# Kernel optimization log

Measured on AMD Instinct MI355X. Metric: run time of the kernel, lower is better.

Reference implementation:

```python
import jax, jax.numpy as jnp
import numpy as np

NE = 20000      # num_ents
NR = 250        # num_rels
R2 = 2 * NR     # num_rels * 2
H = 256         # h_dim
T = 3           # sequence_len (history length)
E = 150000      # edges per timestep
M = 200000      # r_to_e entries per timestep
NNZ_E = 320000  # hypergraph-ent nnz
NNZ_R = 8000    # hypergraph-rel nnz
NLH_E = 2       # n_layers_hypergraph_ent
NLH_R = 2       # n_layers_hypergraph_rel
CH = 50         # ConvTransE channels
NT = 2000       # test triples (doubled with inverses)


def seg_mean(vals, ids, n):
    s = jax.ops.segment_sum(vals, ids, num_segments=n)
    c = jax.ops.segment_sum(jnp.ones((ids.shape[0], 1), vals.dtype), ids, num_segments=n)
    return s / jnp.maximum(c, 1.0)


def l2norm(x, eps=1e-12):  # F.normalize(dim=1)
    n = jnp.linalg.norm(x, axis=-1, keepdims=True)
    return x / jnp.maximum(n, eps)


def gru_cell(x, h, W_ih, W_hh, b_ih, b_hh):  # torch.nn.GRUCell math
    gi = x @ W_ih.T + b_ih
    gh = h @ W_hh.T + b_hh
    i_r, i_z, i_n = jnp.split(gi, 3, axis=-1)
    h_r, h_z, h_n = jnp.split(gh, 3, axis=-1)
    r = jax.nn.sigmoid(i_r + h_r)
    z = jax.nn.sigmoid(i_z + h_z)
    n = jnp.tanh(i_n + r * h_n)
    return (1.0 - z) * n + z * h


def setup_inputs() -> dict:
    key = jax.random.key(0)
    ks = jax.random.split(key, 32)
    inp = {}
    inp['dynamic_emb'] = jax.random.normal(ks[0], (NE, H), jnp.float32)
    inp['emb_rel'] = jax.random.normal(ks[1], (R2, H), jnp.float32) * 0.06
    inp['gru_W_ih'] = jax.random.normal(ks[2], (3 * H, 2 * H), jnp.float32) * 0.05
    inp['gru_W_hh'] = jax.random.normal(ks[3], (3 * H, H), jnp.float32) * 0.05
    inp['gru_b_ih'] = jnp.zeros((3 * H,), jnp.float32)
    inp['gru_b_hh'] = jnp.zeros((3 * H,), jnp.float32)
    inp['agg_W'] = jax.random.normal(ks[4], (H, H), jnp.float32) * 0.06
    inp['tg_W'] = jax.random.normal(ks[5], (H, H), jnp.float32) * 0.06
    inp['tg_b'] = jnp.zeros((H,), jnp.float32)
    inp['hyper_ent_val'] = jax.random.uniform(ks[6], (NNZ_E,), jnp.float32) * (1.0 / 16.0)
    inp['hyper_rel_val'] = jax.random.uniform(ks[7], (NNZ_R,), jnp.float32) * (1.0 / 16.0)
    inp['conv_w'] = jax.random.normal(ks[8], (CH, 3, 3), jnp.float32) * 0.1
    inp['conv_b'] = jnp.zeros((CH,), jnp.float32)
    inp['fc_W'] = jax.random.normal(ks[9], (CH * H, H), jnp.float32) * 0.01
    inp['fc_b'] = jnp.zeros((H,), jnp.float32)
    inp['sentence_emb'] = jax.random.normal(ks[10], (NT, H), jnp.float32)
    inp['edge_src'] = jax.random.randint(ks[11], (T, E), 0, NE, jnp.int64)
    inp['edge_rel'] = jax.random.randint(ks[12], (T, E), 0, R2, jnp.int64)
    inp['edge_dst'] = jax.random.randint(ks[13], (T, E), 0, NE, jnp.int64)
    inp['r_to_e'] = jax.random.randint(ks[14], (T, M), 0, NE, jnp.int64)
    inp['r_ids'] = jax.random.randint(ks[15], (T, M), 0, R2, jnp.int64)
    inp['hyper_ent_row'] = jax.random.randint(ks[16], (NNZ_E,), 0, NE, jnp.int64)
    inp['hyper_ent_col'] = jax.random.randint(ks[17], (NNZ_E,), 0, NE, jnp.int64)
    inp['hyper_rel_row'] = jax.random.randint(ks[18], (NNZ_R,), 0, R2, jnp.int64)
    inp['hyper_rel_col'] = jax.random.randint(ks[19], (NNZ_R,), 0, R2, jnp.int64)
    inp['test_triples'] = jax.random.randint(ks[20], (NT, 3), 0, NR, jnp.int64)
    return inp


def reference(dynamic_emb, emb_rel, gru_W_ih, gru_W_hh, gru_b_ih, gru_b_hh,
              agg_W, tg_W, tg_b, hyper_ent_val, hyper_rel_val,
              conv_w, conv_b, fc_W, fc_b, sentence_emb,
              edge_src, edge_rel, edge_dst, r_to_e, r_ids,
              hyper_ent_row, hyper_ent_col, hyper_rel_row, hyper_rel_col,
              test_triples):
    ent = dynamic_emb   # [NE, H]  (layer_norm=False -> no normalize)
    rel = emb_rel       # [R2, H]
    # --- temporal evolution over history (sequence_len timesteps) ---
    for t in range(T):
        # per-relation gather-mean of involved entity embeddings (r_to_e spans)
        x_mean = seg_mean(ent[r_to_e[t]], r_ids[t], R2)          # [R2, H]
        x_in = jnp.concatenate([rel, x_mean], axis=1)             # [R2, 2H]
        rel = gru_cell(x_in, rel, gru_W_ih, gru_W_hh, gru_b_ih, gru_b_hh)
        # aggregator: relational message passing (mean over in-edges)
        msg = (ent[edge_src[t]] + rel[edge_rel[t]]) @ agg_W       # [E, H]
        curr = jax.nn.relu(seg_mean(msg, edge_dst[t], NE))        # [NE, H]
        # time gate
        tw = jax.nn.sigmoid(ent @ tg_W + tg_b)
        ent = tw * curr + (1.0 - tw) * ent
    # --- hypergraph propagation (sparse spmv + L2 normalize + residual) ---
    x = ent
    for _ in range(NLH_E):
        y = jax.ops.segment_sum(hyper_ent_val[:, None] * x[hyper_ent_col],
                                hyper_ent_row, num_segments=NE)
        x = l2norm(y) + x
    ent = x
    x = rel
    for _ in range(NLH_R):
        y = jax.ops.segment_sum(hyper_rel_val[:, None] * x[hyper_rel_col],
                                hyper_rel_row, num_segments=R2)
        x = l2norm(y) + x
    rel = x
    # --- predict: add inverse triples, ConvTransE decoder ---
    inv = jnp.stack([test_triples[:, 2], test_triples[:, 1] + NR, test_triples[:, 0]], axis=1)
    all_t = jnp.concatenate([test_triples, inv], axis=0)          # [2NT, 3]
    sent = jnp.concatenate([sentence_emb, sentence_emb], axis=0)  # [2NT, H]
    e1 = ent[all_t[:, 0]]
    r1 = rel[all_t[:, 1]]
    feat = jnp.stack([e1, r1, sent], axis=1)                      # [B, 3, H]
    conv = jax.lax.conv_general_dilated(feat, conv_w, window_strides=(1,),
                                        padding=((1, 1),),
                                        dimension_numbers=('NCH', 'OIH', 'NCH'))
    conv = jax.nn.relu(conv + conv_b[None, :, None])              # [B, CH, H]
    q = jax.nn.relu(conv.reshape(feat.shape[0], CH * H) @ fc_W + fc_b)  # [B, H]
    scores = q @ ent.T                                            # [B, NE]
    # cross-entropy over object entity
    tgt = all_t[:, 2]
    logz = jax.scipy.special.logsumexp(scores, axis=1)
    nll = logz - jnp.take_along_axis(scores, tgt[:, None], axis=1)[:, 0]
    return jnp.mean(nll)
```

## Files before the change

### kernel.cpp

```cpp
#include <hip/hip_runtime.h>
#include <math.h>

#define DEV_INLINE __device__ __forceinline__

constexpr int H      = 256;
constexpr int NE     = 20000;
constexpr int NR     = 250;
constexpr int R2     = 500;
constexpr int TT     = 3;
constexpr int NEDGE  = 150000;
constexpr int M      = 200000;
constexpr int NNZ_E  = 320000;
constexpr int NNZ_R  = 8000;
constexpr int CH     = 50;
constexpr int NT     = 2000;
constexpr int NT2    = 4000;
constexpr int H3     = 3 * H;
constexpr int KFC    = CH * H;
constexpr int ROWPAD = 4096;
constexpr int NCHUNK = 32;
constexpr int SPP    = 20;
constexpr int MSPLIT = 8;
constexpr int FSPLIT = 20;
constexpr int NB_CS  = 64;
constexpr int NEPAD  = 20480;
constexpr int NB_NE  = 80;
constexpr float PADCOLS = 480.f;

constexpr int CNT_NE_BASE   = 2048;
constexpr int CNT_NE_STRIDE = 20224;
constexpr int CNT_TOTAL     = CNT_NE_BASE + 4 * CNT_NE_STRIDE;

typedef __bf16 bf16x8 __attribute__((ext_vector_type(8)));
typedef float  f32x4  __attribute__((ext_vector_type(4)));

DEV_INLINE bf16x8 ldb8(const __bf16* p) { return *(const bf16x8*)p; }
DEV_INLINE bf16x8 zerob8() { uint4 z = make_uint4(0, 0, 0, 0); return __builtin_bit_cast(bf16x8, z); }
DEV_INLINE f32x4 mfma16(bf16x8 a, bf16x8 b, f32x4 c) {
  return __builtin_amdgcn_mfma_f32_16x16x32_bf16(a, b, c, 0, 0, 0);
}
DEV_INLINE void gload_lds16(const void* g, void* l) {
  __builtin_amdgcn_global_load_lds((const __attribute__((address_space(1))) void*)g,
                                   (__attribute__((address_space(3))) void*)l, 16, 0, 0);
}

DEV_INLINE float block_sum256(float v) {
  __shared__ float ws[4];
  #pragma unroll
  for (int o = 32; o > 0; o >>= 1) v += __shfl_down(v, o, 64);
  if ((threadIdx.x & 63) == 0) ws[threadIdx.x >> 6] = v;
  __syncthreads();
  float r = ws[0] + ws[1] + ws[2] + ws[3];
  __syncthreads();
  return r;
}

__global__ void cs_hist_k(const int* __restrict__ r_ids, const int* __restrict__ hr_row,
                          int* __restrict__ bcnt)
{
  __shared__ int lh[512];
  int a = blockIdx.y;
  const int* keys = (a < 3) ? r_ids + (size_t)a * M : hr_row;
  int n = (a < 3) ? M : NNZ_R;
  int t = threadIdx.x;
  lh[t] = 0; lh[t + 256] = 0;
  __syncthreads();
  int chunk = (n + NB_CS - 1) / NB_CS;
  int i0 = blockIdx.x * chunk, i1 = min(i0 + chunk, n);
  for (int i = i0 + t; i < i1; i += 256) atomicAdd(&lh[keys[i]], 1);
  __syncthreads();
  int* outp = bcnt + ((size_t)a * NB_CS + blockIdx.x) * 512;
  outp[t] = lh[t]; outp[t + 256] = lh[t + 256];
}

__global__ void cs_scan_k(const int* __restrict__ bcnt, int* __restrict__ bbase,
                          int* __restrict__ start_all)
{
  __shared__ int ps[257];
  int a = blockIdx.x;
  int* start = start_all + ((a < 3) ? a * 512 : 1536);
  const int* bc = bcnt + (size_t)a * NB_CS * 512;
  int* bb = bbase + (size_t)a * NB_CS * 512;
  int t = threadIdx.x;
  int b0 = 2 * t, b1 = 2 * t + 1;
  int tot0 = 0, tot1 = 0;
  for (int blk = 0; blk < NB_CS; blk++) {
    tot0 += bc[blk * 512 + b0];
    tot1 += bc[blk * 512 + b1];
  }
  ps[t + 1] = tot0 + tot1;
  if (t == 0) ps[0] = 0;
  __syncthreads();
  if (t == 0) { for (int i = 1; i <= 256; i++) ps[i] += ps[i - 1]; }
  __syncthreads();
  int run0 = ps[t], run1 = ps[t] + tot0;
  start[b0] = run0;
  start[b1] = run1;
  for (int blk = 0; blk < NB_CS; blk++) {
    bb[blk * 512 + b0] = run0; run0 += bc[blk * 512 + b0];
    bb[blk * 512 + b1] = run1; run1 += bc[blk * 512 + b1];
  }
}

__global__ void cs_scatter_k(const int* __restrict__ r_ids, const int* __restrict__ r_to_e,
                             const int* __restrict__ hr_row, const int* __restrict__ hr_col,
                             const float* __restrict__ hrv, const int* __restrict__ bbase,
                             int* __restrict__ f0, int* __restrict__ f1, int* __restrict__ f2,
                             int2* __restrict__ fcvHR)
{
  __shared__ int cur[512];
  int a = blockIdx.y;
  const int* keys = (a < 3) ? r_ids + (size_t)a * M : hr_row;
  int n = (a < 3) ? M : NNZ_R;
  int t = threadIdx.x;
  const int* bb = bbase + ((size_t)a * NB_CS + blockIdx.x) * 512;
  cur[t] = bb[t]; cur[t + 256] = bb[t + 256];
  __syncthreads();
  int chunk = (n + NB_CS - 1) / NB_CS;
  int i0 = blockIdx.x * chunk, i1 = min(i0 + chunk, n);
  if (a < 3) {
    const int* other = r_to_e + (size_t)a * M;
    int* f = (a == 0) ? f0 : (a == 1) ? f1 : f2;
    for (int i = i0 + t; i < i1; i += 256) {
      int p = atomicAdd(&cur[keys[i]], 1);
      f[p] = other[i];
    }
  } else {
    for (int i = i0 + t; i < i1; i += 256) {
      int p = atomicAdd(&cur[keys[i]], 1);
      fcvHR[p] = make_int2(hr_col[i], __float_as_int(hrv[i]));
    }
  }
}

__global__ void hist_ne_k(const int* __restrict__ edge_dst, const int* __restrict__ he_row,
                          int* __restrict__ cnt_all)
{
  int a = blockIdx.y;
  const int* keys = (a < 3) ? edge_dst + (size_t)a * NEDGE : he_row;
  int n = (a < 3) ? NEDGE : NNZ_E;
  int* cnt = cnt_all + CNT_NE_BASE + a * CNT_NE_STRIDE;
  int i = blockIdx.x * 256 + threadIdx.x;
  if (i < n) atomicAdd(&cnt[keys[i]], 1);
}

__global__ void scan_ne1_k(const int* __restrict__ cnt_all, int* __restrict__ start_all,
                           int* __restrict__ bsum)
{
  __shared__ int wtot[4];
  int a = blockIdx.y;
  int off = CNT_NE_BASE + a * CNT_NE_STRIDE;
  int bin = blockIdx.x * 256 + threadIdx.x;
  int lane = threadIdx.x & 63, w = threadIdx.x >> 6;
  int v = (bin < NE) ? cnt_all[off + bin] : 0;
  int orig = v;
  #pragma unroll
  for (int o = 1; o < 64; o <<= 1) {
    int n = __shfl_up(v, o, 64);
    if (lane >= o) v += n;
  }
  if (lane == 63) wtot[w] = v;
  __syncthreads();
  int wo = 0;
  #pragma unroll
  for (int i = 0; i < 4; i++) if (i < w) wo += wtot[i];
  if (bin < NE) start_all[off + bin] = v - orig + wo;
  if (threadIdx.x == 255) bsum[a * NB_NE + blockIdx.x] = wo + v;
}

__global__ void scan_ne2_k(int* __restrict__ bsum, int* __restrict__ start_all)
{
  __shared__ int s[NB_NE + 1];
  int a = blockIdx.x;
  int t = threadIdx.x;
  if (t < NB_NE) s[t + 1] = bsum[a * NB_NE + t];
  if (t == 0) s[0] = 0;
  __syncthreads();
  if (t == 0) { for (int i = 1; i <= NB_NE; i++) s[i] += s[i - 1]; }
  __syncthreads();
  if (t < NB_NE) bsum[a * NB_NE + t] = s[t];
  if (t == 0) start_all[CNT_NE_BASE + a * CNT_NE_STRIDE + NE] = s[NB_NE];
}

__global__ void scan_ne3_k(int* __restrict__ start_all, int* __restrict__ cursor_all,
                           const int* __restrict__ bsum)
{
  int a = blockIdx.y;
  int off = CNT_NE_BASE + a * CNT_NE_STRIDE;
  int bin = blockIdx.x * 256 + threadIdx.x;
  if (bin >= NE) return;
  int v = start_all[off + bin] + bsum[a * NB_NE + blockIdx.x];
  start_all[off + bin] = v;
  cursor_all[off + bin] = v;
}

__global__ void perm_fuse2i_k(const int* __restrict__ edge_dst, const int* __restrict__ edge_src,
                              const int* __restrict__ edge_rel, int* __restrict__ cursor_all,
                              int2* __restrict__ f0, int2* __restrict__ f1, int2* __restrict__ f2)
{
  int a = blockIdx.y;
  const int* keys = edge_dst + (size_t)a * NEDGE;
  const int* o1 = edge_src + (size_t)a * NEDGE;
  const int* o2 = edge_rel + (size_t)a * NEDGE;
  int* cursor = cursor_all + CNT_NE_BASE + a * CNT_NE_STRIDE;
  int2* f = (a == 0) ? f0 : (a == 1) ? f1 : f2;
  int i = blockIdx.x * 256 + threadIdx.x;
  if (i < NEDGE) { int p = atomicAdd(&cursor[keys[i]], 1); f[p] = make_int2(o1[i], o2[i]); }
}
__global__ void perm_fusevi_k(const int* __restrict__ keys, const int* __restrict__ col,
                              const float* __restrict__ val, int n, int* __restrict__ cursor,
                              int2* __restrict__ f)
{
  int i = blockIdx.x * 256 + threadIdx.x;
  if (i < n) {
    int p = atomicAdd(&cursor[keys[i]], 1);
    f[p] = make_int2(col[i], __float_as_int(val[i]));
  }
}

__global__ void cast_bf16_k(const float* __restrict__ in, __bf16* __restrict__ out, int n8)
{
  int i = blockIdx.x * 256 + threadIdx.x;
  if (i >= n8) return;
  const float4* p = (const float4*)in + (size_t)i * 2;
  float4 u = p[0], v = p[1];
  bf16x8 o;
  o[0] = (__bf16)u.x; o[1] = (__bf16)u.y; o[2] = (__bf16)u.z; o[3] = (__bf16)u.w;
  o[4] = (__bf16)v.x; o[5] = (__bf16)v.y; o[6] = (__bf16)v.z; o[7] = (__bf16)v.w;
  ((bf16x8*)out)[i] = o;
}

__global__ void copy_cast_k(const float* __restrict__ in, float* __restrict__ outf,
                            __bf16* __restrict__ outb, int n8)
{
  int i = blockIdx.x * 256 + threadIdx.x;
  if (i >= n8) return;
  const float4* p = (const float4*)in + (size_t)i * 2;
  float4 u = p[0], v = p[1];
  ((float4*)outf)[(size_t)i * 2]     = u;
  ((float4*)outf)[(size_t)i * 2 + 1] = v;
  bf16x8 o;
  o[0] = (__bf16)u.x; o[1] = (__bf16)u.y; o[2] = (__bf16)u.z; o[3] = (__bf16)u.w;
  o[4] = (__bf16)v.x; o[5] = (__bf16)v.y; o[6] = (__bf16)v.z; o[7] = (__bf16)v.w;
  ((bf16x8*)outb)[i] = o;
}

__global__ void transpose_cast_k(const float* __restrict__ in, __bf16* __restrict__ out,
                                 int K, int N)
{
  __shared__ float tile[32][33];
  int tx = threadIdx.x & 31, ty = threadIdx.x >> 5;
  int kb = blockIdx.x * 32, nb = blockIdx.y * 32;
  #pragma unroll
  for (int i = 0; i < 4; i++)
    tile[ty + i * 8][tx] = in[(size_t)(kb + ty + i * 8) * N + nb + tx];
  __syncthreads();
  #pragma unroll
  for (int i = 0; i < 4; i++)
    out[(size_t)(nb + ty + i * 8) * K + kb + tx] = (__bf16)tile[tx][ty + i * 8];
}

__global__ void pack_frag_k(const __bf16* __restrict__ src, __bf16* __restrict__ dst,
                            int nchunks, int Mr)
{
  int i = blockIdx.x * 256 + threadIdx.x;
  if (i >= nchunks) return;
  int c = i >> 5, s = i & 31;
  bf16x8 v = (c < Mr) ? ldb8(src + (size_t)c * H + s * 8) : zerob8();
  int kf = s >> 2, kg = s & 3;
  size_t d = ((((size_t)(c >> 6) * 4 + ((c >> 4) & 3)) * 8 + kf) * 4 + kg) * 16 + (c & 15);
  *(bf16x8*)(dst + d * 8) = v;
}

__global__ void gather_mean2_k(const __bf16* __restrict__ src, const int* __restrict__ fidx,
                               const int* __restrict__ start, float* __restrict__ part)
{
  __shared__ __align__(16) float red[4][H];
  int r = blockIdx.x, s = blockIdx.y;
  int s0 = start[r], s1 = start[r + 1];
  int len = s1 - s0;
  int chunk = (len + MSPLIT - 1) / MSPLIT;
  int jb = s0 + s * chunk, je = min(jb + chunk, s1);
  int tid = threadIdx.x, lane = tid & 63, w = tid >> 6;
  int half = lane >> 5, l = lane & 31;
  float acc[8] = {0.f, 0.f, 0.f, 0.f, 0.f, 0.f, 0.f, 0.f};
  for (int j = jb + w * 2 + half; j < je; j += 8) {
    int e = fidx[j];
    bf16x8 v = ldb8(src + (size_t)e * H + l * 8);
    #pragma unroll
    for (int q = 0; q < 8; q++) acc[q] += (float)v[q];
  }
  #pragma unroll
  for (int q = 0; q < 8; q++) acc[q] += __shfl_xor(acc[q], 32, 64);
  if (half == 0) {
    *(float4*)&red[w][l * 8]     = make_float4(acc[0], acc[1], acc[2], acc[3]);
    *(float4*)&red[w][l * 8 + 4] = make_float4(acc[4], acc[5], acc[6], acc[7]);
  }
  __syncthreads();
  int h = tid;
  part[((size_t)r * MSPLIT + s) * H + h] = red[0][h] + red[1][h] + red[2][h] + red[3][h];
}

__global__ void mean_xin_k(const float* __restrict__ partM, const int* __restrict__ start,
                           const float* __restrict__ rel, __bf16* __restrict__ xin)
{
  int r = blockIdx.x, h = threadIdx.x;
  float s = 0.f;
  #pragma unroll
  for (int z = 0; z < MSPLIT; z++) s += partM[((size_t)r * MSPLIT + z) * H + h];
  float xm = s / (float)max(start[r + 1] - start[r], 1);
  xin[(size_t)r * 2 * H + h]     = (__bf16)rel[(size_t)r * H + h];
  xin[(size_t)r * 2 * H + H + h] = (__bf16)xm;
}

__global__ void gather_edges3_k(const __bf16* __restrict__ ent, const __bf16* __restrict__ rel,
                                const int2* __restrict__ fsr,
                                const int* __restrict__ start, __bf16* __restrict__ out)
{
  __shared__ __align__(16) float red[4][H];
  int d = blockIdx.x;
  int s0 = start[d], s1 = start[d + 1];
  int tid = threadIdx.x, lane = tid & 63, w = tid >> 6;
  int half = lane >> 5, l = lane & 31;
  const __bf16* srcbase = half ? rel : ent;
  float acc[8] = {0.f, 0.f, 0.f, 0.f, 0.f, 0.f, 0.f, 0.f};
  for (int j = s0 + w; j < s1; j += 4) {
    int2 e2 = fsr[j];
    int e = half ? e2.y : e2.x;
    bf16x8 v = ldb8(srcbase + (size_t)e * H + l * 8);
    #pragma unroll
    for (int q = 0; q < 8; q++) acc[q] += (float)v[q];
  }
  #pragma unroll
  for (int q = 0; q < 8; q++) acc[q] += __shfl_xor(acc[q], 32, 64);
  if (half == 0) {
    *(float4*)&red[w][l * 8]     = make_float4(acc[0], acc[1], acc[2], acc[3]);
    *(float4*)&red[w][l * 8 + 4] = make_float4(acc[4], acc[5], acc[6], acc[7]);
  }
  __syncthreads();
  int h = tid;
  float sum = red[0][h] + red[1][h] + red[2][h] + red[3][h];
  out[(size_t)d * H + h] = (__bf16)(sum / (float)max(s1 - s0, 1));
}

__global__ void hyper3_k(const float* __restrict__ x, const __bf16* __restrict__ xb,
                         const int2* __restrict__ fcv,
                         const int* __restrict__ start,
                         float* __restrict__ xout, __bf16* __restrict__ xoutb)
{
  __shared__ __align__(16) float red[4][H];
  int r = blockIdx.x;
  int s0 = start[r], s1 = start[r + 1];
  int tid = threadIdx.x, lane = tid & 63, w = tid >> 6;
  int half = lane >> 5, l = lane & 31;
  float acc[8] = {0.f, 0.f, 0.f, 0.f, 0.f, 0.f, 0.f, 0.f};
  for (int j = s0 + w * 2 + half; j < s1; j += 8) {
    int2 cv = fcv[j];
    float wt = __int_as_float(cv.y);
    bf16x8 v = ldb8(xb + (size_t)cv.x * H + l * 8);
    #pragma unroll
    for (int q = 0; q < 8; q++) acc[q] += wt * (float)v[q];
  }
  #pragma unroll
  for (int q = 0; q < 8; q++) acc[q] += __shfl_xor(acc[q], 32, 64);
  if (half == 0) {
    *(float4*)&red[w][l * 8]     = make_float4(acc[0], acc[1], acc[2], acc[3]);
    *(float4*)&red[w][l * 8 + 4] = make_float4(acc[4], acc[5], acc[6], acc[7]);
  }
  __syncthreads();
  int h = tid;
  float y = red[0][h] + red[1][h] + red[2][h] + red[3][h];
  float ss = block_sum256(y * y);
  float rn = 1.f / fmaxf(sqrtf(ss), 1e-12f);
  float o = x[(size_t)r * H + h] + y * rn;
  xout[(size_t)r * H + h] = o;
  xoutb[(size_t)r * H + h] = (__bf16)o;
}

__global__ void hyper_rel_k(const float* __restrict__ x, const int2* __restrict__ fcv,
                            const int* __restrict__ start, float* __restrict__ xout)
{
  int r = blockIdx.x, h = threadIdx.x;
  int s0 = start[r], s1 = start[r + 1];
  float a0 = 0.f;
  for (int j = s0; j < s1; j++) {
    int2 cv = fcv[j];
    a0 += __int_as_float(cv.y) * x[(size_t)cv.x * H + h];
  }
  float ss = block_sum256(a0 * a0);
  float rn = 1.f / fmaxf(sqrtf(ss), 1e-12f);
  xout[(size_t)r * H + h] = x[(size_t)r * H + h] + a0 * rn;
}

__global__ void gru_combine(const float* __restrict__ gi, const float* __restrict__ gh,
                            float* __restrict__ rel, __bf16* __restrict__ relb)
{
  int idx = blockIdx.x * 256 + threadIdx.x;
  if (idx >= R2 * H) return;
  int i = idx >> 8, h = idx & 255;
  const float* gir = gi + (size_t)i * H3;
  const float* ghr = gh + (size_t)i * H3;
  float r = 1.f / (1.f + __expf(-(gir[h]       + ghr[h])));
  float z = 1.f / (1.f + __expf(-(gir[H + h]   + ghr[H + h])));
  float n = tanhf(gir[2 * H + h] + r * ghr[2 * H + h]);
  float o = (1.f - z) * n + z * rel[idx];
  rel[idx] = o;
  relb[idx] = (__bf16)o;
}

DEV_INLINE void stage64_load(uint4* v, const __bf16* src, int rowBase, int rowLimit, int tid)
{
  #pragma unroll
  for (int q = 0; q < 8; q++) {
    int X = (q * 256 + tid) * 16;
    int row = X >> 9, boff = X & 511;
    int grow = min(rowBase + row, rowLimit);
    v[q] = *(const uint4*)((const char*)src + (size_t)grow * 512 + boff);
  }
}
DEV_INLINE void stage64_write(char* lds, const uint4* v, int tid)
{
  #pragma unroll
  for (int q = 0; q < 8; q++) {
    int X = (q * 256 + tid) * 16;
    int row = X >> 9;
    *(uint4*)(lds + (X ^ ((row & 7) << 4))) = v[q];
  }
}
DEV_INLINE bf16x8 frag64(const char* lds, int row, int kf, int kg)
{
  int off = (kf * 64 + kg * 16) ^ ((row & 7) << 4);
  return *(const bf16x8*)(lds + row * 512 + off);
}

template<int EPI>
__global__ __launch_bounds__(256, 2) void panel2_gemm(const __bf16* __restrict__ A,
                                                      const __bf16* __restrict__ B,
                                                      const float* __restrict__ bias,
                                                      float* __restrict__ out,
                                                      int Mr, int N,
                                                      const float* __restrict__ gate,
                                                      float* __restrict__ entf,
                                                      __bf16* __restrict__ entbo)
{
  __shared__ __attribute__((aligned(16))) char lds0[32768];
  __shared__ __attribute__((aligned(16))) char lds1[32768];
  int tid = threadIdx.x;
  int lane = tid & 63, wM = tid >> 6;
  int r = lane & 15, kg = lane >> 4;
  int rowBase = blockIdx.y * 128;

  {
    uint4 va[8];
    stage64_load(va, A, rowBase, Mr - 1, tid);
    stage64_write(lds0, va, tid);
    stage64_load(va, A, rowBase + 64, Mr - 1, tid);
    stage64_write(lds1, va, tid);
  }
  __syncthreads();

  bf16x8 a[2][8];
  {
    int base = wM * 32;
    const char* ab = (base >= 64) ? lds1 : lds0;
    #pragma unroll
    for (int i = 0; i < 2; i++) {
      int ar = (base + i * 16 + r) & 63;
      #pragma unroll
      for (int kf = 0; kf < 8; kf++) a[i][kf] = frag64(ab, ar, kf, kg);
    }
  }
  __syncthreads();
  {
    uint4 va[8];
    stage64_load(va, B, blockIdx.x * 64, N - 1, tid);
    stage64_write(lds0, va, tid);
  }
  __syncthreads();

  f32x4 acc[2][4];
  #pragma unroll
  for (int i = 0; i < 2; i++)
    #pragma unroll
    for (int j = 0; j < 4; j++) {
      acc[i][j][0] = 0.f; acc[i][j][1] = 0.f; acc[i][j][2] = 0.f; acc[i][j][3] = 0.f;
    }
  __builtin_amdgcn_s_setprio(1);
  #pragma unroll
  for (int kf = 0; kf < 8; kf++) {
    bf16x8 b[4];
    #pragma unroll
    for (int j = 0; j < 4; j++) b[j] = frag64(lds0, j * 16 + r, kf, kg);
    #pragma unroll
    for (int i = 0; i < 2; i++)
      #pragma unroll
      for (int j = 0; j < 4; j++)
        acc[i][j] = mfma16(a[i][kf], b[j], acc[i][j]);
  }
  __builtin_amdgcn_s_setprio(0);

  #pragma unroll
  for (int i = 0; i < 2; i++)
    #pragma unroll
    for (int g = 0; g < 4; g++) {
      int row = rowBase + wM * 32 + i * 16 + kg * 4 + g;
      if (row >= Mr) continue;
      #pragma unroll
      for (int j = 0; j < 4; j++) {
        int col = blockIdx.x * 64 + j * 16 + r;
        if (col >= N) continue;
        float v = acc[i][j][g];
        if (EPI == 2) {
          if (bias) v += bias[col];
          v = 1.f / (1.f + __expf(-v));
          out[(size_t)row * N + col] = v;
        } else {
          v = fmaxf(v, 0.f);
          size_t idx = (size_t)row * N + col;
          float t = gate[idx];
          float o = t * v + (1.f - t) * entf[idx];
          entf[idx] = o;
          entbo[idx] = (__bf16)o;
        }
      }
    }
}

__global__ __launch_bounds__(256, 3) void scores_v4(const __bf16* __restrict__ qbf,
                                                    const __bf16* __restrict__ ebf,
                                                    float* __restrict__ part_l)
{
  __shared__ __attribute__((aligned(16))) char lds[2][16384];
  int tid = threadIdx.x, lane = tid & 63, w = tid >> 6;
  int r = lane & 15, kg = lane >> 4;

  auto stage = [&](int buf, int p) {
    const char* g = (const char*)ebf + ((size_t)(blockIdx.x * SPP + p)) * 16384;
    int wbase = (tid & ~63) * 16;
    #pragma unroll
    for (int q = 0; q < 4; q++) {
      int o = q * 4096 + wbase;
      gload_lds16(g + o + lane * 16, lds[buf] + o);
    }
  };

  stage(0, 0);

  bf16x8 a[2][8];
  {
    int cb = blockIdx.y * 2 + (w >> 1);
    int jb = (w & 1) * 2;
    const __bf16* ap = qbf + (size_t)cb * 16384 + kg * 128 + r * 8;
    #pragma unroll
    for (int i = 0; i < 2; i++)
      #pragma unroll
      for (int kf = 0; kf < 8; kf++)
        a[i][kf] = ldb8(ap + ((jb + i) * 8 + kf) * 512);
  }
  __syncthreads();

  float lsum[2][4];
  #pragma unroll
  for (int i = 0; i < 2; i++)
    #pragma unroll
    for (int g = 0; g < 4; g++) lsum[i][g] = 0.f;

  const char* l0 = lds[0] + kg * 256 + r * 16;
  const char* l1 = lds[1] + kg * 256 + r * 16;

  for (int p = 0; p < SPP; p++) {
    if (p + 1 < SPP) stage((p + 1) & 1, p + 1);
    const char* cur = (p & 1) ? l1 : l0;

    f32x4 acc[2][2];
    #pragma unroll
    for (int i = 0; i < 2; i++)
      #pragma unroll
      for (int j = 0; j < 2; j++) {
        acc[i][j][0] = 0.f; acc[i][j][1] = 0.f; acc[i][j][2] = 0.f; acc[i][j][3] = 0.f;
      }
    __builtin_amdgcn_s_setprio(1);
    #pragma unroll
    for (int kf = 0; kf < 8; kf++) {
      bf16x8 b0 = *(const bf16x8*)(cur + (0 * 8 + kf) * 1024);
      bf16x8 b1 = *(const bf16x8*)(cur + (1 * 8 + kf) * 1024);
      acc[0][0] = mfma16(a[0][kf], b0, acc[0][0]);
      acc[0][1] = mfma16(a[0][kf], b1, acc[0][1]);
      acc[1][0] = mfma16(a[1][kf], b0, acc[1][0]);
      acc[1][1] = mfma16(a[1][kf], b1, acc[1][1]);
    }
    __builtin_amdgcn_s_setprio(0);

    #pragma unroll
    for (int j = 0; j < 2; j++)
      #pragma unroll
      for (int i = 0; i < 2; i++)
        #pragma unroll
        for (int g = 0; g < 4; g++)
          lsum[i][g] += exp2f(acc[i][j][g]);
    __syncthreads();
  }

  #pragma unroll
  for (int m = 1; m < 16; m <<= 1)
    #pragma unroll
    for (int i = 0; i < 2; i++)
      #pragma unroll
      for (int g = 0; g < 4; g++)
        lsum[i][g] += __shfl_xor(lsum[i][g], m, 64);
  if (r == 0) {
    #pragma unroll
    for (int i = 0; i < 2; i++)
      #pragma unroll
      for (int g = 0; g < 4; g++) {
        int row = blockIdx.y * 128 + w * 32 + i * 16 + kg * 4 + g;
        part_l[(size_t)blockIdx.x * ROWPAD + row] = lsum[i][g];
      }
  }
}

__global__ __launch_bounds__(256) void fc_gemm(const __bf16* __restrict__ A,
                                               const __bf16* __restrict__ Bt,
                                               float* __restrict__ part, int Mr)
{
  __shared__ __attribute__((aligned(16))) char lds[49152];
  int tid = threadIdx.x;
  int lane = tid & 63, wave = tid >> 6;
  int wM = wave >> 1, wN = wave & 1;
  int r = lane & 15, kg = lane >> 4;
  int rowBase = blockIdx.y * 128;
  int kbeg = blockIdx.x * (KFC / FSPLIT);

  f32x4 acc[4][8];
  #pragma unroll
  for (int i = 0; i < 4; i++)
    #pragma unroll
    for (int j = 0; j < 8; j++) {
      acc[i][j][0] = 0.f; acc[i][j][1] = 0.f; acc[i][j][2] = 0.f; acc[i][j][3] = 0.f;
    }

  for (int ks = 0; ks < KFC / FSPLIT / 64; ks++) {
    int kb = kbeg + ks * 64;
    #pragma unroll
    for (int q = 0; q < 12; q++) {
      int X = (q * 256 + tid) * 16;
      int row = X >> 7;
      int off = X & 127;
      int soff = off ^ ((row & 7) << 4);
      uint4 v;
      if (row < 128) {
        int grow = min(rowBase + row, Mr - 1);
        v = *(const uint4*)((const char*)A + (size_t)grow * (KFC * 2) + kb * 2 + soff);
      } else {
        int col = row - 128;
        v = *(const uint4*)((const char*)Bt + (size_t)col * (KFC * 2) + kb * 2 + soff);
      }
      *(uint4*)(lds + X) = v;
    }
    __syncthreads();
    #pragma unroll
    for (int kf = 0; kf < 2; kf++) {
      bf16x8 a[4], b[8];
      #pragma unroll
      for (int i = 0; i < 4; i++) {
        int row = wM * 64 + i * 16 + r;
        int off = (kf * 64 + kg * 16) ^ ((row & 7) << 4);
        a[i] = *(const bf16x8*)(lds + row * 128 + off);
      }
      #pragma unroll
      for (int j = 0; j < 8; j++) {
        int row = 128 + wN * 128 + j * 16 + r;
        int off = (kf * 64 + kg * 16) ^ ((row & 7) << 4);
        b[j] = *(const bf16x8*)(lds + row * 128 + off);
      }
      #pragma unroll
      for (int i = 0; i < 4; i++)
        #pragma unroll
        for (int j = 0; j < 8; j++)
          acc[i][j] = mfma16(a[i], b[j], acc[i][j]);
    }
    __syncthreads();
  }

  float* pz = part + (size_t)blockIdx.x * Mr * H;
  #pragma unroll
  for (int i = 0; i < 4; i++)
    #pragma unroll
    for (int g = 0; g < 4; g++) {
      int row = rowBase + wM * 64 + i * 16 + kg * 4 + g;
      if (row >= Mr) continue;
      #pragma unroll
      for (int j = 0; j < 8; j++) {
        int col = wN * 128 + j * 16 + r;
        pz[(size_t)row * H + col] = acc[i][j][g];
      }
    }
}

__global__ void gru_gemm2_k(const __bf16* __restrict__ xinb, const __bf16* __restrict__ relb,
                            const __bf16* __restrict__ Wihb, const __bf16* __restrict__ Whhb,
                            const float* __restrict__ b_ih, const float* __restrict__ b_hh,
                            float* __restrict__ gi, float* __restrict__ gh)
{
  const __bf16* A; const __bf16* Bt; const float* bias; float* C; int K;
  if (blockIdx.z == 0) { A = xinb; Bt = Wihb; bias = b_ih; C = gi; K = 2 * H; }
  else                 { A = relb; Bt = Whhb; bias = b_hh; C = gh; K = H; }
  const int Mr = R2, N = H3;

  int lane = threadIdx.x & 63, wave = threadIdx.x >> 6;
  int waveM = wave >> 1, waveN = wave & 1;
  int r = lane & 15, kg = lane >> 4;
  int rowBase = blockIdx.y * 64 + waveM * 32;
  int colBase = blockIdx.x * 64 + waveN * 32;

  int row0 = rowBase + r, row1 = rowBase + 16 + r;
  int col0 = colBase + r, col1 = colBase + 16 + r;
  bool v0 = row0 < Mr, v1 = row1 < Mr;
  const __bf16* a0p = A + (size_t)row0 * K + kg * 8;
  const __bf16* a1p = A + (size_t)row1 * K + kg * 8;
  const __bf16* b0p = Bt + (size_t)col0 * K + kg * 8;
  const __bf16* b1p = Bt + (size_t)col1 * K + kg * 8;

  f32x4 acc[2][2];
  #pragma unroll
  for (int i = 0; i < 2; i++)
    #pragma unroll
    for (int j = 0; j < 2; j++) { acc[i][j][0] = 0.f; acc[i][j][1] = 0.f; acc[i][j][2] = 0.f; acc[i][j][3] = 0.f; }

  for (int k0 = 0; k0 < K; k0 += 32) {
    bf16x8 a0 = v0 ? ldb8(a0p + k0) : zerob8();
    bf16x8 a1 = v1 ? ldb8(a1p + k0) : zerob8();
    bf16x8 b0 = ldb8(b0p + k0);
    bf16x8 b1 = ldb8(b1p + k0);
    acc[0][0] = mfma16(a0, b0, acc[0][0]);
    acc[0][1] = mfma16(a0, b1, acc[0][1]);
    acc[1][0] = mfma16(a1, b0, acc[1][0]);
    acc[1][1] = mfma16(a1, b1, acc[1][1]);
  }

  #pragma unroll
  for (int i = 0; i < 2; i++) {
    #pragma unroll
    for (int g = 0; g < 4; g++) {
      int row = rowBase + i * 16 + kg * 4 + g;
      if (row >= Mr) continue;
      #pragma unroll
      for (int j = 0; j < 2; j++) {
        int col = colBase + j * 16 + r;
        C[(size_t)row * N + col] = acc[i][j][g] + bias[col];
      }
    }
  }
}

__global__ void fc_reduce(const float* __restrict__ part, const float* __restrict__ bias,
                          float* __restrict__ q, __bf16* __restrict__ qb, int nrows)
{
  int idx = blockIdx.x * 256 + threadIdx.x;
  if (idx >= nrows * H) return;
  int col = idx & 255;
  float s = bias[col];
  for (int z = 0; z < FSPLIT; z++) s += part[(size_t)z * nrows * H + idx];
  s = fmaxf(s, 0.f);
  q[idx] = s;
  qb[idx] = (__bf16)(s * 1.44269504f);
}

__global__ void conv_feat(const float* __restrict__ ent, const float* __restrict__ rel,
                          const float* __restrict__ sent, const int* __restrict__ tt,
                          const float* __restrict__ cw, const float* __restrict__ cb,
                          __bf16* __restrict__ out, int row0)
{
  __shared__ float f[3][258];
  __shared__ float wsm[CH * 9];
  __shared__ float bsm[CH];
  int i = row0 + blockIdx.x;
  int h = threadIdx.x;
  int j = (i < NT) ? i : i - NT;
  int a0 = (i < NT) ? tt[j * 3 + 0] : tt[j * 3 + 2];
  int a1 = (i < NT) ? tt[j * 3 + 1] : tt[j * 3 + 1] + NR;
  f[0][h + 1] = ent[(size_t)a0 * H + h];
  f[1][h + 1] = rel[(size_t)a1 * H + h];
  f[2][h + 1] = sent[(size_t)j * H + h];
  if (h < 3) { f[h][0] = 0.f; f[h][257] = 0.f; }
  for (int x = h; x < CH * 9; x += 256) wsm[x] = cw[x];
  if (h < CH) bsm[h] = cb[h];
  __syncthreads();
  __bf16* orow = out + (size_t)blockIdx.x * KFC;
  for (int c = 0; c < CH; c++) {
    const float* wc = wsm + c * 9;
    float s = bsm[c];
    #pragma unroll
    for (int ic = 0; ic < 3; ic++)
      s += wc[ic * 3 + 0] * f[ic][h] + wc[ic * 3 + 1] * f[ic][h + 1] + wc[ic * 3 + 2] * f[ic][h + 2];
    orow[(size_t)c * H + h] = (__bf16)fmaxf(s, 0.f);
  }
}

__global__ void lse_combine(const float* __restrict__ part_l, const float* __restrict__ qf,
                            const float* __restrict__ ent, const int* __restrict__ tt,
                            float* __restrict__ nll)
{
  int gid = blockIdx.x * 256 + threadIdx.x;
  int w = gid >> 6;
  if (w >= NT2) return;
  int lane = gid & 63;
  int j = (w < NT) ? w : w - NT;
  int tgt = (w < NT) ? tt[j * 3 + 2] : tt[j * 3 + 0];
  const float4 qa = ((const float4*)(qf + (size_t)w * H))[lane];
  const float4 ea = ((const float4*)(ent + (size_t)tgt * H))[lane];
  float d = qa.x * ea.x + qa.y * ea.y + qa.z * ea.z + qa.w * ea.w;
  float s = (lane < NCHUNK) ? part_l[(size_t)lane * ROWPAD + w] : 0.f;
  #pragma unroll
  for (int o = 32; o > 0; o >>= 1) {
    d += __shfl_down(d, o, 64);
    s += __shfl_down(s, o, 64);
  }
  if (lane == 0) nll[w] = logf(s - PADCOLS) - d;
}

__global__ void mean_nll(const float* __restrict__ nll, float* __restrict__ out)
{
  float s = 0.f;
  for (int i = threadIdx.x; i < NT2; i += 256) s += nll[i];
  s = block_sum256(s);
  if (threadIdx.x == 0) out[0] = s * (1.f / NT2);
}

extern "C" void kernel_launch(void* const* d_in, const int* in_sizes, int n_in,
                              void* d_out, int out_size, void* d_ws, size_t ws_size,
                              hipStream_t stream)
{
  const float* dynamic_emb = (const float*)d_in[0];
  const float* emb_rel     = (const float*)d_in[1];
  const float* gru_W_ih    = (const float*)d_in[2];
  const float* gru_W_hh    = (const float*)d_in[3];
  const float* gru_b_ih    = (const float*)d_in[4];
  const float* gru_b_hh    = (const float*)d_in[5];
  const float* agg_W       = (const float*)d_in[6];
  const float* tg_W        = (const float*)d_in[7];
  const float* tg_b        = (const float*)d_in[8];
  const float* hev         = (const float*)d_in[9];
  const float* hrv         = (const float*)d_in[10];
  const float* conv_w      = (const float*)d_in[11];
  const float* conv_b      = (const float*)d_in[12];
  const float* fc_W        = (const float*)d_in[13];
  const float* fc_b        = (const float*)d_in[14];
  const float* sent        = (const float*)d_in[15];
  const int* edge_src = (const int*)d_in[16];
  const int* edge_rel = (const int*)d_in[17];
  const int* edge_dst = (const int*)d_in[18];
  const int* r_to_e   = (const int*)d_in[19];
  const int* r_ids    = (const int*)d_in[20];
  const int* he_row   = (const int*)d_in[21];
  const int* he_col   = (const int*)d_in[22];
  const int* hr_row   = (const int*)d_in[23];
  const int* hr_col   = (const int*)d_in[24];
  const int* tt       = (const int*)d_in[25];
  float* out = (float*)d_out;

  char* base = (char*)d_ws;
  size_t off = 0;
  auto alloc = [&](size_t bytes) { char* p = base + off; off += (bytes + 255) & ~(size_t)255; return p; };

  float* ent    = (float*)alloc((size_t)NE * H * 4);
  float* curr   = (float*)alloc((size_t)NE * H * 4);
  float* tgbuf  = (float*)alloc((size_t)NE * H * 4);
  __bf16* convb = (__bf16*)curr;
  __bf16* entb  = (__bf16*)alloc((size_t)NE * H * 2);
  __bf16* entb2 = (__bf16*)alloc((size_t)NE * H * 2);
  __bf16* accEb = (__bf16*)alloc((size_t)NE * H * 2);
  __bf16* ebf   = (__bf16*)alloc((size_t)NEPAD * H * 2);
  __bf16* qbf   = (__bf16*)alloc((size_t)ROWPAD * H * 2);
  float* rel    = (float*)alloc((size_t)R2 * H * 4);
  float* accR   = (float*)alloc((size_t)R2 * H * 4);
  __bf16* relb  = (__bf16*)alloc((size_t)R2 * H * 2);
  __bf16* xinb  = (__bf16*)alloc((size_t)R2 * 2 * H * 2);
  float* gi     = (float*)alloc((size_t)R2 * H3 * 4);
  float* gh     = (float*)alloc((size_t)R2 * H3 * 4);
  float* qf     = (float*)alloc((size_t)NT2 * H * 4);
  __bf16* qb    = (__bf16*)alloc((size_t)NT2 * H * 2);
  float* part_l = (float*)alloc((size_t)NCHUNK * ROWPAD * 4);
  float* partM  = (float*)alloc((size_t)R2 * MSPLIT * H * 4);
  float* fcpart = (float*)alloc((size_t)FSPLIT * 1600 * H * 4);
  float* nll    = (float*)alloc((size_t)NT2 * 4);
  __bf16* tgWtb = (__bf16*)alloc((size_t)H * H * 2);
  __bf16* aggWtb= (__bf16*)alloc((size_t)H * H * 2);
  __bf16* fcWtb = (__bf16*)alloc((size_t)H * KFC * 2);
  __bf16* Wihb  = (__bf16*)alloc((size_t)H3 * 2 * H * 2);
  __bf16* Whhb  = (__bf16*)alloc((size_t)H3 * H * 2);

  int* ip = (int*)alloc(0);
  size_t ioff = 0;
  auto ialloc = [&](size_t n) { int* p = ip + ioff; ioff += n; return p; };
  int* fidxM[TT];
  int2* fsrE[TT];
  for (int t = 0; t < TT; t++) fidxM[t] = ialloc(M);
  for (int t = 0; t < TT; t++) fsrE[t] = (int2*)ialloc((size_t)NEDGE * 2);
  int2* fcvHE = (int2*)ialloc((size_t)NNZ_E * 2);
  int2* fcvHR = (int2*)ialloc((size_t)NNZ_R * 2);
  int* cnt_all    = ialloc(CNT_TOTAL);
  int* start_all  = ialloc(CNT_TOTAL);
  int* cursor_all = ialloc(CNT_TOTAL);
  int* bcnt  = ialloc((size_t)4 * NB_CS * 512);
  int* bbase = ialloc((size_t)4 * NB_CS * 512);
  int* bsumNE = ialloc((size_t)4 * NB_NE);

  int* sM[TT];  for (int t = 0; t < TT; t++) sM[t] = start_all + t * 512;
  int* sHR = start_all + 1536;
  int* sE[TT];  for (int t = 0; t < TT; t++) sE[t] = start_all + CNT_NE_BASE + t * CNT_NE_STRIDE;
  int* sHE = start_all + CNT_NE_BASE + 3 * CNT_NE_STRIDE;

  transpose_cast_k<<<dim3(H / 32, H / 32), 256, 0, stream>>>(tg_W, tgWtb, H, H);
  transpose_cast_k<<<dim3(H / 32, H / 32), 256, 0, stream>>>(agg_W, aggWtb, H, H);
  transpose_cast_k<<<dim3(KFC / 32, H / 32), 256, 0, stream>>>(fc_W, fcWtb, KFC, H);
  cast_bf16_k<<<(H3 * 2 * H / 8 + 255) / 256, 256, 0, stream>>>(gru_W_ih, Wihb, H3 * 2 * H / 8);
  cast_bf16_k<<<(H3 * H / 8 + 255) / 256, 256, 0, stream>>>(gru_W_hh, Whhb, H3 * H / 8);

  cs_hist_k<<<dim3(NB_CS, 4), 256, 0, stream>>>(r_ids, hr_row, bcnt);
  cs_scan_k<<<4, 256, 0, stream>>>(bcnt, bbase, start_all);
  cs_scatter_k<<<dim3(NB_CS, 4), 256, 0, stream>>>(r_ids, r_to_e, hr_row, hr_col, hrv, bbase,
                                                   fidxM[0], fidxM[1], fidxM[2], fcvHR);

  hipMemsetAsync(cnt_all + CNT_NE_BASE, 0, (size_t)(CNT_TOTAL - CNT_NE_BASE) * 4, stream);
  hist_ne_k<<<dim3((NNZ_E + 255) / 256, 4), 256, 0, stream>>>(edge_dst, he_row, cnt_all);
  scan_ne1_k<<<dim3(NB_NE, 4), 256, 0, stream>>>(cnt_all, start_all, bsumNE);
  scan_ne2_k<<<4, 256, 0, stream>>>(bsumNE, start_all);
  scan_ne3_k<<<dim3(NB_NE, 4), 256, 0, stream>>>(start_all, cursor_all, bsumNE);
  perm_fuse2i_k<<<dim3((NEDGE + 255) / 256, 3), 256, 0, stream>>>(
      edge_dst, edge_src, edge_rel, cursor_all, fsrE[0], fsrE[1], fsrE[2]);
  perm_fusevi_k<<<(NNZ_E + 255) / 256, 256, 0, stream>>>(
      he_row, he_col, hev, NNZ_E, cursor_all + CNT_NE_BASE + 3 * CNT_NE_STRIDE, fcvHE);

  constexpr int NEH8 = NE * H / 8, R2H8 = R2 * H / 8;
  constexpr int NE_RB = (NE + 127) / 128;

  copy_cast_k<<<(NEH8 + 255) / 256, 256, 0, stream>>>(dynamic_emb, ent, entb, NEH8);
  copy_cast_k<<<(R2H8 + 255) / 256, 256, 0, stream>>>(emb_rel, rel, relb, R2H8);

  for (int t = 0; t < TT; t++) {
    gather_mean2_k<<<dim3(R2, MSPLIT), 256, 0, stream>>>(entb, fidxM[t], sM[t], partM);
    mean_xin_k<<<R2, 256, 0, stream>>>(partM, sM[t], rel, xinb);
    gru_gemm2_k<<<dim3(H3 / 64, (R2 + 63) / 64, 2), 256, 0, stream>>>(
        xinb, relb, Wihb, Whhb, gru_b_ih, gru_b_hh, gi, gh);
    gru_combine<<<(R2 * H + 255) / 256, 256, 0, stream>>>(gi, gh, rel, relb);

    panel2_gemm<2><<<dim3(4, NE_RB), 256, 0, stream>>>(
        entb, tgWtb, tg_b, tgbuf, NE, H, nullptr, nullptr, nullptr);
    gather_edges3_k<<<NE, 256, 0, stream>>>(entb, relb, fsrE[t], sE[t], accEb);
    panel2_gemm<4><<<dim3(4, NE_RB), 256, 0, stream>>>(
        accEb, aggWtb, nullptr, nullptr, NE, H, tgbuf, ent, entb);
  }

  hyper3_k<<<NE, 256, 0, stream>>>(ent, entb, fcvHE, sHE, curr, entb2);
  hyper3_k<<<NE, 256, 0, stream>>>(curr, entb2, fcvHE, sHE, ent, entb);
  hyper_rel_k<<<R2, 256, 0, stream>>>(rel, fcvHR, sHR, accR);
  hyper_rel_k<<<R2, 256, 0, stream>>>(accR, fcvHR, sHR, rel);

  pack_frag_k<<<(NEPAD * 32 + 255) / 256, 256, 0, stream>>>(entb, ebf, NEPAD * 32, NE);

  for (int c = 0; c < 3; c++) {
    int row0 = c * 1600;
    int rows = min(1600, NT2 - row0);
    conv_feat<<<rows, 256, 0, stream>>>(ent, rel, sent, tt, conv_w, conv_b, convb, row0);
    fc_gemm<<<dim3(FSPLIT, (rows + 127) / 128), 256, 0, stream>>>(convb, fcWtb, fcpart, rows);
    fc_reduce<<<(rows * H + 255) / 256, 256, 0, stream>>>(
        fcpart, fc_b, qf + (size_t)row0 * H, qb + (size_t)row0 * H, rows);
  }

  pack_frag_k<<<(ROWPAD * 32 + 255) / 256, 256, 0, stream>>>(qb, qbf, ROWPAD * 32, NT2);

  scores_v4<<<dim3(NCHUNK, 32), 256, 0, stream>>>(qbf, ebf, part_l);
  lse_combine<<<(NT2 * 64 + 255) / 256, 256, 0, stream>>>(part_l, qf, ent, tt, nll);
  mean_nll<<<1, 256, 0, stream>>>(nll, out);
}
```

Measured before the change: 801.2 us.

## Use direct global-to-LDS loads and double-buffer the FC GEMM K loop

Tile staging in panel2_gemm and fc_gemm now uses direct global-to-LDS 16-byte loads (gload_lds16) instead of loading into registers and then writing to LDS. The swizzle moves from the LDS destination to the global source address. fc_gemm also gains a second LDS buffer so the next K-slice is prefetched while MFMA runs on the current one, with setprio raised around the compute. This aims to hide global load latency and cut VGPR pressure, at the cost of twice the LDS in fc_gemm (96KB), which may lower occupancy.

New measurement: 776.1 us (median of 2 runs). 3.1% less time.

```diff
diff --git a/kernel.cpp b/kernel.cpp
--- a/kernel.cpp
+++ b/kernel.cpp
@@ -408,23 +408,17 @@
   relb[idx] = (__bf16)o;
 }
 
-DEV_INLINE void stage64_load(uint4* v, const __bf16* src, int rowBase, int rowLimit, int tid)
-{
+DEV_INLINE void stage64_g(const __bf16* src, char* lds, int rowBase, int rowLimit, int tid)
+{
+  int lane = tid & 63;
+  int wbase = (tid & ~63) * 16;
   #pragma unroll
   for (int q = 0; q < 8; q++) {
-    int X = (q * 256 + tid) * 16;
+    int X = q * 4096 + wbase + lane * 16;
     int row = X >> 9, boff = X & 511;
+    int soff = boff ^ ((row & 7) << 4);
     int grow = min(rowBase + row, rowLimit);
-    v[q] = *(const uint4*)((const char*)src + (size_t)grow * 512 + boff);
-  }
-}
-DEV_INLINE void stage64_write(char* lds, const uint4* v, int tid)
-{
-  #pragma unroll
-  for (int q = 0; q < 8; q++) {
-    int X = (q * 256 + tid) * 16;
-    int row = X >> 9;
-    *(uint4*)(lds + (X ^ ((row & 7) << 4))) = v[q];
+    gload_lds16((const char*)src + (size_t)grow * 512 + soff, lds + q * 4096 + wbase);
   }
 }
 DEV_INLINE bf16x8 frag64(const char* lds, int row, int kf, int kg)
@@ -450,13 +444,8 @@
   int r = lane & 15, kg = lane >> 4;
   int rowBase = blockIdx.y * 128;
 
-  {
-    uint4 va[8];
-    stage64_load(va, A, rowBase, Mr - 1, tid);
-    stage64_write(lds0, va, tid);
-    stage64_load(va, A, rowBase + 64, Mr - 1, tid);
-    stage64_write(lds1, va, tid);
-  }
+  stage64_g(A, lds0, rowBase, Mr - 1, tid);
+  stage64_g(A, lds1, rowBase + 64, Mr - 1, tid);
   __syncthreads();
 
   bf16x8 a[2][8];
@@ -471,11 +460,7 @@
     }
   }
   __syncthreads();
-  {
-    uint4 va[8];
-    stage64_load(va, B, blockIdx.x * 64, N - 1, tid);
-    stage64_write(lds0, va, tid);
-  }
+  stage64_g(B, lds0, blockIdx.x * 64, N - 1, tid);
   __syncthreads();
 
   f32x4 acc[2][4];
@@ -623,13 +608,32 @@
                                                const __bf16* __restrict__ Bt,
                                                float* __restrict__ part, int Mr)
 {
-  __shared__ __attribute__((aligned(16))) char lds[49152];
+  __shared__ __attribute__((aligned(16))) char lds[2][49152];
   int tid = threadIdx.x;
   int lane = tid & 63, wave = tid >> 6;
   int wM = wave >> 1, wN = wave & 1;
   int r = lane & 15, kg = lane >> 4;
   int rowBase = blockIdx.y * 128;
   int kbeg = blockIdx.x * (KFC / FSPLIT);
+  int wbase = (tid & ~63) * 16;
+
+  auto stage = [&](int buf, int ks) {
+    int kb = kbeg + ks * 64;
+    #pragma unroll
+    for (int q = 0; q < 12; q++) {
+      int X = q * 4096 + wbase + lane * 16;
+      int row = X >> 7, off = X & 127;
+      int soff = off ^ ((row & 7) << 4);
+      const char* g;
+      if (row < 128) {
+        int grow = min(rowBase + row, Mr - 1);
+        g = (const char*)A + (size_t)grow * (KFC * 2) + kb * 2 + soff;
+      } else {
+        g = (const char*)Bt + (size_t)(row - 128) * (KFC * 2) + kb * 2 + soff;
+      }
+      gload_lds16(g, lds[buf] + q * 4096 + wbase);
+    }
+  };
 
   f32x4 acc[4][8];
   #pragma unroll
@@ -639,25 +643,14 @@
       acc[i][j][0] = 0.f; acc[i][j][1] = 0.f; acc[i][j][2] = 0.f; acc[i][j][3] = 0.f;
     }
 
-  for (int ks = 0; ks < KFC / FSPLIT / 64; ks++) {
-    int kb = kbeg + ks * 64;
-    #pragma unroll
-    for (int q = 0; q < 12; q++) {
-      int X = (q * 256 + tid) * 16;
-      int row = X >> 7;
-      int off = X & 127;
-      int soff = off ^ ((row & 7) << 4);
-      uint4 v;
-      if (row < 128) {
-        int grow = min(rowBase + row, Mr - 1);
-        v = *(const uint4*)((const char*)A + (size_t)grow * (KFC * 2) + kb * 2 + soff);
-      } else {
-        int col = row - 128;
-        v = *(const uint4*)((const char*)Bt + (size_t)col * (KFC * 2) + kb * 2 + soff);
-      }
-      *(uint4*)(lds + X) = v;
-    }
-    __syncthreads();
+  constexpr int NS = KFC / FSPLIT / 64;
+  stage(0, 0);
+  __syncthreads();
+
+  for (int ks = 0; ks < NS; ks++) {
+    if (ks + 1 < NS) stage((ks + 1) & 1, ks + 1);
+    const char* L = lds[ks & 1];
+    __builtin_amdgcn_s_setprio(1);
     #pragma unroll
     for (int kf = 0; kf < 2; kf++) {
       bf16x8 a[4], b[8];
@@ -665,13 +658,13 @@
       for (int i = 0; i < 4; i++) {
         int row = wM * 64 + i * 16 + r;
         int off = (kf * 64 + kg * 16) ^ ((row & 7) << 4);
-        a[i] = *(const bf16x8*)(lds + row * 128 + off);
+        a[i] = *(const bf16x8*)(L + row * 128 + off);
       }
       #pragma unroll
       for (int j = 0; j < 8; j++) {
         int row = 128 + wN * 128 + j * 16 + r;
         int off = (kf * 64 + kg * 16) ^ ((row & 7) << 4);
-        b[j] = *(const bf16x8*)(lds + row * 128 + off);
+        b[j] = *(const bf16x8*)(L + row * 128 + off);
       }
       #pragma unroll
       for (int i = 0; i < 4; i++)
@@ -679,6 +672,7 @@
         for (int j = 0; j < 8; j++)
           acc[i][j] = mfma16(a[i], b[j], acc[i][j]);
     }
+    __builtin_amdgcn_s_setprio(0);
     __syncthreads();
   }
 
```
